# Performance work log

Hardware: AMD Instinct MI355X
Metric: run time of the kernel (lower is better)

The kernel has to match this reference:

```python
import jax, jax.numpy as jnp
import numpy as np

B, C, H, W = 4, 512, 128, 128
CI = C // 2   # inter_planes
CQ = C // 8   # q/k dim in CrossAttention


def conv1x1(x, w, b=None):
    # x: [B,Cin,H,W], w: [Cout,Cin]
    y = jnp.einsum('oc,bchw->bohw', w, x)
    if b is not None:
        y = y + b[None, :, None, None]
    return y


def setup_inputs() -> dict:
    key = jax.random.key(0)
    ks = jax.random.split(key, 13)
    s = 0.05
    return {
        'x': jax.random.normal(ks[0], (B, C, H, W), jnp.float32),
        # SCCA gating params (1x1 convs, no bias except conv_up)
        'w_q_right': jax.random.normal(ks[1], (1, C), jnp.float32) * s,
        'w_v_right': jax.random.normal(ks[2], (CI, C), jnp.float32) * s,
        'w_up': jax.random.normal(ks[3], (C, CI), jnp.float32) * s,
        'b_up': jnp.zeros((C,), jnp.float32),
        'w_q_left': jax.random.normal(ks[4], (CI, C), jnp.float32) * s,
        'w_v_left': jax.random.normal(ks[5], (CI, C), jnp.float32) * s,
        # CrossAttention params (1x1 convs with bias)
        'wq': jax.random.normal(ks[6], (CQ, C), jnp.float32) * s,
        'bq': jnp.zeros((CQ,), jnp.float32),
        'wk': jax.random.normal(ks[7], (CQ, C), jnp.float32) * s,
        'bk': jnp.zeros((CQ,), jnp.float32),
        'wv': jax.random.normal(ks[8], (C, C), jnp.float32) * s,
        'bv': jnp.zeros((C,), jnp.float32),
        'gamma': jnp.asarray(0.5, jnp.float32),
    }


def cross_attention(x, wq, bq, wk, bk, wv, bv, gamma):
    # criss-cross attention: each pixel attends to its row and column
    b, c, h, w = x.shape
    q = conv1x1(x, wq, bq)   # [B,CQ,H,W]
    k = conv1x1(x, wk, bk)   # [B,CQ,H,W]
    v = conv1x1(x, wv, bv)   # [B,C,H,W]
    # column (H) affinities with -inf on the self diagonal (as in INF())
    diag = jnp.where(jnp.eye(h, dtype=bool), -jnp.inf, 0.0).astype(x.dtype)
    e_h = jnp.einsum('bchw,bcgw->bhwg', q, k) + diag[None, :, None, :]  # [B,H,W,H]
    e_w = jnp.einsum('bchw,bchv->bhwv', q, k)                            # [B,H,W,W]
    att = jax.nn.softmax(jnp.concatenate([e_h, e_w], axis=-1), axis=-1)  # [B,H,W,H+W]
    a_h, a_w = att[..., :h], att[..., h:]
    out_h = jnp.einsum('bcgw,bhwg->bchw', v, a_h)
    out_w = jnp.einsum('bchv,bhwv->bchw', v, a_w)
    return gamma * (out_h + out_w) + x


def spatial_weighted(x, w_q_right, w_v_right, w_up, b_up):
    b, c, h, w = x.shape
    input_x = conv1x1(x, w_v_right).reshape(b, CI, h * w)       # [B,CI,HW]
    mask = jax.nn.softmax(conv1x1(x, w_q_right).reshape(b, h * w), axis=-1)  # [B,HW]
    ctx = jnp.einsum('bcn,bn->bc', input_x, mask)               # [B,CI]
    ctx = jnp.einsum('oc,bc->bo', w_up, ctx) + b_up             # [B,C]
    mask_ch = jax.nn.sigmoid(ctx)[:, :, None, None]
    return x * mask_ch


def channel_weighted(x, w_q_left, w_v_left):
    b, c, h, w = x.shape
    g_x = conv1x1(x, w_q_left)                                  # [B,CI,H,W]
    avg = g_x.mean(axis=(2, 3))                                 # [B,CI]
    theta = conv1x1(x, w_v_left).reshape(b, CI, h * w)          # [B,CI,HW]
    ctx = jax.nn.softmax(jnp.einsum('bc,bcn->bn', avg, theta), axis=-1)
    mask_sp = jax.nn.sigmoid(ctx).reshape(b, 1, h, w)
    return x * mask_sp


def reference(x, w_q_right, w_v_right, w_up, b_up, w_q_left, w_v_left,
              wq, bq, wk, bk, wv, bv, gamma):
    cc = spatial_weighted(x, w_q_right, w_v_right, w_up, b_up)
    cc = cross_attention(cc, wq, bq, wk, bk, wv, bv, gamma)
    cs = channel_weighted(x, w_q_left, w_v_left)
    cs = cross_attention(cs, wq, bq, wk, bk, wv, bv, gamma)
    out = cs + cc
    out = cross_attention(out, wq, bq, wk, bk, wv, bv, gamma)
    return out
```

## Files before the change

kernel.cpp:

```cpp
#include <hip/hip_runtime.h>
#include <hip/hip_bf16.h>
#include <math.h>

typedef __hip_bfloat16 bf16;
typedef __attribute__((ext_vector_type(8))) short s16x8;
typedef __attribute__((ext_vector_type(4))) float f32x4;

constexpr int Bn  = 4;
constexpr int Cn  = 512;
constexpr int Hn  = 128;
constexpr int Wn  = 128;
constexpr int Nn  = Hn * Wn;
constexpr int CQn = 64;
constexpr int CIn = 256;

__device__ __forceinline__ float bf2f(bf16 v){ return __bfloat162float(v); }
__device__ __forceinline__ bf16  f2bf(float v){ return __float2bfloat16(v); }

__device__ __forceinline__ void gload_lds16(const void* g, void* l){
  __builtin_amdgcn_global_load_lds(
      (const __attribute__((address_space(1))) unsigned int*)g,
      (__attribute__((address_space(3))) unsigned int*)l,
      16, 0, 0);
}


__global__ __launch_bounds__(256) void k_dotc(const float* __restrict__ x,
                                              const float* __restrict__ w,
                                              int wstride,
                                              float* __restrict__ out){
  int t = blockIdx.x * 256 + threadIdx.x;
  int b = t >> 14;
  const float* wp = w + (size_t)b * wstride;
  const float* xp = x + (size_t)b * Cn * Nn + (t & (Nn - 1));
  float acc = 0.f;
  #pragma unroll 8
  for (int c = 0; c < Cn; ++c) acc += wp[c] * xp[(size_t)c * Nn];
  out[t] = acc;
}

__global__ __launch_bounds__(256) void k_rowmean(const float* __restrict__ x,
                                                 float* __restrict__ out,
                                                 float scale){
  int bc = blockIdx.x;
  const float* xp = x + (size_t)bc * Nn;
  float acc = 0.f;
  for (int n = threadIdx.x; n < Nn; n += 256) acc += xp[n];
  for (int o = 32; o > 0; o >>= 1) acc += __shfl_down(acc, o);
  __shared__ float red[4];
  if ((threadIdx.x & 63) == 0) red[threadIdx.x >> 6] = acc;
  __syncthreads();
  if (threadIdx.x == 0) out[bc] = (red[0] + red[1] + red[2] + red[3]) * scale;
}

__global__ __launch_bounds__(256) void k_rowdot(const float* __restrict__ W,
                                                const float* __restrict__ vec,
                                                float* __restrict__ out){
  __shared__ float vs[Cn];
  int b = blockIdx.x, t = threadIdx.x;
  for (int j = t; j < Cn; j += 256) vs[j] = vec[b * Cn + j];
  __syncthreads();
  const float4* wp = (const float4*)(W + (size_t)t * Cn);
  float a = 0.f;
  #pragma unroll 4
  for (int j = 0; j < Cn / 4; ++j){
    float4 w4 = wp[j];
    a += w4.x * vs[4*j] + w4.y * vs[4*j+1] + w4.z * vs[4*j+2] + w4.w * vs[4*j+3];
  }
  out[b * CIn + t] = a;
}

__global__ __launch_bounds__(256) void k_coldot(const float* __restrict__ W,
                                                const float* __restrict__ vec,
                                                float* __restrict__ out){
  __shared__ float vs[CIn];
  int b = blockIdx.y, t = threadIdx.x;
  int c = blockIdx.x * 256 + t;
  if (t < CIn) vs[t] = vec[b * CIn + t];
  __syncthreads();
  float a = 0.f;
  #pragma unroll 8
  for (int j = 0; j < CIn; ++j) a += W[(size_t)j * Cn + c] * vs[j];
  out[b * Cn + c] = a;
}

__global__ __launch_bounds__(256) void k_mch2(const float* __restrict__ w_up,
                                              const float* __restrict__ b_up,
                                              const float* __restrict__ ctx,
                                              float* __restrict__ mch){
  __shared__ float cs[CIn];
  int b = blockIdx.y, t = threadIdx.x;
  int o = blockIdx.x * 256 + t;
  if (t < CIn) cs[t] = ctx[b * CIn + t];
  __syncthreads();
  const float4* wp = (const float4*)(w_up + (size_t)o * CIn);
  float a = b_up[o];
  #pragma unroll 4
  for (int j = 0; j < CIn / 4; ++j){
    float4 w4 = wp[j];
    a += w4.x * cs[4*j] + w4.y * cs[4*j+1] + w4.z * cs[4*j+2] + w4.w * cs[4*j+3];
  }
  mch[b * Cn + o] = 1.f / (1.f + expf(-a));
}

__global__ __launch_bounds__(1024) void k_stats(const float* __restrict__ vv,
                                                float* __restrict__ stats){
  int b = blockIdx.x;
  const float* pp = vv + (size_t)b * Nn;
  int t = threadIdx.x;
  float m = -3.4e38f;
  for (int n = t; n < Nn; n += 1024) m = fmaxf(m, pp[n]);
  for (int o = 32; o > 0; o >>= 1) m = fmaxf(m, __shfl_down(m, o));
  __shared__ float red[16];
  int wid = t >> 6, lid = t & 63;
  if (lid == 0) red[wid] = m;
  __syncthreads();
  if (t == 0){
    float q = red[0];
    for (int i = 1; i < 16; i++) q = fmaxf(q, red[i]);
    red[0] = q;
  }
  __syncthreads();
  m = red[0];
  __syncthreads();
  float s = 0.f;
  for (int n = t; n < Nn; n += 1024) s += expf(pp[n] - m);
  for (int o = 32; o > 0; o >>= 1) s += __shfl_down(s, o);
  if (lid == 0) red[wid] = s;
  __syncthreads();
  if (t == 0){
    float q = 0.f;
    for (int i = 0; i < 16; i++) q += red[i];
    stats[b * 2]     = m;
    stats[b * 2 + 1] = q;
  }
}

__global__ __launch_bounds__(256) void k_weighted(const float* __restrict__ x,
                                                  const float* __restrict__ logits,
                                                  const float* __restrict__ stats,
                                                  float* __restrict__ out){
  int bc = blockIdx.x;
  int b = bc >> 9;
  const float* xp = x + (size_t)bc * Nn;
  const float* lp = logits + (size_t)b * Nn;
  float m = stats[b * 2], den = stats[b * 2 + 1];
  float acc = 0.f;
  for (int n = threadIdx.x; n < Nn; n += 256) acc += xp[n] * expf(lp[n] - m);
  for (int o = 32; o > 0; o >>= 1) acc += __shfl_down(acc, o);
  __shared__ float red[4];
  if ((threadIdx.x & 63) == 0) red[threadIdx.x >> 6] = acc;
  __syncthreads();
  if (threadIdx.x == 0) out[bc] = (red[0] + red[1] + red[2] + red[3]) / den;
}

__global__ __launch_bounds__(256) void k_msp(const float* __restrict__ lg,
                                             const float* __restrict__ stats,
                                             float* __restrict__ msp){
  int t = blockIdx.x * 256 + threadIdx.x;
  int b = t >> 14;
  float v = expf(lg[t] - stats[b * 2]) / stats[b * 2 + 1];
  msp[t] = 1.f / (1.f + expf(-v));
}

__global__ __launch_bounds__(256) void k_applyT(const float* __restrict__ x,
                                                const float* __restrict__ mch,
                                                const float* __restrict__ msp,
                                                float* __restrict__ cc,
                                                float* __restrict__ cs,
                                                bf16* __restrict__ out_hi,
                                                bf16* __restrict__ out_lo){
  __shared__ bf16 th_[32][33];
  __shared__ bf16 tl_[32][33];
  int nt = blockIdx.x, ct = blockIdx.y, b = blockIdx.z;
  int n0 = nt * 32, c0 = ct * 32;
  int t = threadIdx.x;
  #pragma unroll
  for (int kk = 0; kk < 4; ++kk){
    int idx = t + kk * 256;
    int cl = idx >> 5, nl = idx & 31;
    size_t off = ((size_t)(b * Cn + c0 + cl)) * Nn + n0 + nl;
    float xv = x[off];
    float ccv = xv * mch[b * Cn + c0 + cl];
    float csv = xv * msp[b * Nn + n0 + nl];
    cc[off] = ccv;
    cs[off] = csv;
    bf16 h = f2bf(ccv);
    th_[cl][nl] = h;
    tl_[cl][nl] = f2bf(ccv - bf2f(h));
  }
  __syncthreads();
  #pragma unroll
  for (int kk = 0; kk < 4; ++kk){
    int idx = t + kk * 256;
    int nl = idx >> 5, cl = idx & 31;
    size_t o = ((size_t)(b * Nn + n0 + nl)) * Cn + c0 + cl;
    out_hi[o] = th_[cl][nl];
    out_lo[o] = tl_[cl][nl];
  }
}


__global__ __launch_bounds__(256) void k_cvt_w(const float* __restrict__ in,
                                               bf16* __restrict__ out, int n){
  int t = blockIdx.x * 256 + threadIdx.x;
  if (t < n) out[t] = f2bf(in[t]);
}

__global__ __launch_bounds__(256) void k_prep_wqk(const float* __restrict__ wq,
                                                  const float* __restrict__ wk,
                                                  const float* __restrict__ bq,
                                                  const float* __restrict__ bk,
                                                  bf16* __restrict__ wqk_hi,
                                                  bf16* __restrict__ wqk_lo,
                                                  float* __restrict__ bqk){
  int t = blockIdx.x * 256 + threadIdx.x;
  int o = t >> 9, c = t & 511;
  float v = (o < 64) ? wq[(size_t)o * Cn + c] : wk[(size_t)(o - 64) * Cn + c];
  bf16 h = f2bf(v);
  wqk_hi[t] = h;
  wqk_lo[t] = f2bf(v - bf2f(h));
  if (t < 128) bqk[t] = (t < 64) ? bq[t] : bk[t - 64];
}

__global__ __launch_bounds__(256) void k_cvt_T(const float* __restrict__ in,
                                               bf16* __restrict__ out_hi,
                                               bf16* __restrict__ out_lo){
  __shared__ bf16 th_[32][33];
  __shared__ bf16 tl_[32][33];
  int nt = blockIdx.x, ct = blockIdx.y, b = blockIdx.z;
  int n0 = nt * 32, c0 = ct * 32;
  int t = threadIdx.x;
  #pragma unroll
  for (int kk = 0; kk < 4; ++kk){
    int idx = t + kk * 256;
    int cl = idx >> 5, nl = idx & 31;
    float v = in[((size_t)(b * Cn + c0 + cl)) * Nn + n0 + nl];
    bf16 h = f2bf(v);
    th_[cl][nl] = h;
    tl_[cl][nl] = f2bf(v - bf2f(h));
  }
  __syncthreads();
  #pragma unroll
  for (int kk = 0; kk < 4; ++kk){
    int idx = t + kk * 256;
    int nl = idx >> 5, cl = idx & 31;
    size_t o = ((size_t)(b * Nn + n0 + nl)) * Cn + c0 + cl;
    out_hi[o] = th_[cl][nl];
    out_lo[o] = tl_[cl][nl];
  }
}


__global__ __launch_bounds__(256) void k_v_mfma(const bf16* __restrict__ xT,
                                                const bf16* __restrict__ wvb,
                                                const float* __restrict__ bv,
                                                bf16* __restrict__ v){
  __shared__ short As[128 * 64];
  __shared__ short Bs[128 * 64];
  __shared__ float bvs[128];
  int lin = blockIdx.x;
  int swz = (lin & 7) * 256 + (lin >> 3);
  int cb = (swz & 3) * 128;
  int nb = ((swz >> 2) & 127) * 128;
  int b  = swz >> 9;
  int t = threadIdx.x, lane = t & 63, wid = t >> 6;
  int wm = wid >> 1, wn = wid & 1;
  int l15 = lane & 15, l4 = lane >> 4;
  if (t < 128) bvs[t] = bv[cb + t];
  f32x4 acc[4][4];
  #pragma unroll
  for (int i = 0; i < 4; i++)
    #pragma unroll
    for (int j = 0; j < 4; j++) acc[i][j] = (f32x4){0.f, 0.f, 0.f, 0.f};

  const bf16* wp = wvb + (size_t)cb * Cn;
  const bf16* xp = xT + ((size_t)b * Nn + nb) * Cn;
  int r8 = lane >> 3;
  int kc = (lane & 7) * 8;
  for (int kt = 0; kt < 8; ++kt){
    int k0 = kt * 64;
    #pragma unroll
    for (int j = 0; j < 4; ++j){
      int inst = wid * 4 + j;
      int row = inst * 8 + r8;
      gload_lds16(wp + (size_t)row * Cn + k0 + kc, (char*)As + inst * 1024);
      gload_lds16(xp + (size_t)row * Cn + k0 + kc, (char*)Bs + inst * 1024);
    }
    __syncthreads();
    #pragma unroll
    for (int kk = 0; kk < 64; kk += 32){
      s16x8 a[4], bb[4];
      #pragma unroll
      for (int mi = 0; mi < 4; mi++)
        a[mi] = *(const s16x8*)&As[(wm * 64 + mi * 16 + l15) * 64 + kk + l4 * 8];
      #pragma unroll
      for (int ni = 0; ni < 4; ni++)
        bb[ni] = *(const s16x8*)&Bs[(wn * 64 + ni * 16 + l15) * 64 + kk + l4 * 8];
      #pragma unroll
      for (int mi = 0; mi < 4; mi++)
        #pragma unroll
        for (int ni = 0; ni < 4; ni++)
          acc[mi][ni] = __builtin_amdgcn_mfma_f32_16x16x32_bf16(a[mi], bb[ni], acc[mi][ni], 0, 0, 0);
    }
    __syncthreads();
  }
  #pragma unroll
  for (int mi = 0; mi < 4; mi++){
    #pragma unroll
    for (int r = 0; r < 4; r++){
      int cl = wm * 64 + mi * 16 + l4 * 4 + r;
      int c  = cb + cl;
      float bias = bvs[cl];
      #pragma unroll
      for (int ni = 0; ni < 4; ni++){
        int n = nb + wn * 64 + ni * 16 + l15;
        v[((size_t)(b * Cn + c)) * Nn + n] = f2bf(acc[mi][ni][r] + bias);
      }
    }
  }
}

__global__ __launch_bounds__(256) void k_qk_mfma(const bf16* __restrict__ xT_hi,
                                                 const bf16* __restrict__ xT_lo,
                                                 const bf16* __restrict__ wqk_hi,
                                                 const bf16* __restrict__ wqk_lo,
                                                 const float* __restrict__ bqk,
                                                 bf16* __restrict__ q,
                                                 bf16* __restrict__ k){
  __shared__ short Ah[128 * 64];
  __shared__ short Al[128 * 64];
  __shared__ short Bh[128 * 64];
  __shared__ short Bl[128 * 64];
  __shared__ float bs[128];
  int nb = blockIdx.x * 128, b = blockIdx.y;
  int t = threadIdx.x, lane = t & 63, wid = t >> 6;
  int wm = wid >> 1, wn = wid & 1;
  int l15 = lane & 15, l4 = lane >> 4;
  if (t < 128) bs[t] = bqk[t];
  f32x4 acc[4][4];
  #pragma unroll
  for (int i = 0; i < 4; i++)
    #pragma unroll
    for (int j = 0; j < 4; j++) acc[i][j] = (f32x4){0.f, 0.f, 0.f, 0.f};

  const bf16* xh = xT_hi + ((size_t)b * Nn + nb) * Cn;
  const bf16* xl = xT_lo + ((size_t)b * Nn + nb) * Cn;
  int r8 = lane >> 3;
  int kc = (lane & 7) * 8;
  for (int kt = 0; kt < 8; ++kt){
    int k0 = kt * 64;
    #pragma unroll
    for (int j = 0; j < 4; ++j){
      int inst = wid * 4 + j;
      int row = inst * 8 + r8;
      size_t off = (size_t)row * Cn + k0 + kc;
      gload_lds16(wqk_hi + off, (char*)Ah + inst * 1024);
      gload_lds16(wqk_lo + off, (char*)Al + inst * 1024);
      gload_lds16(xh + off,     (char*)Bh + inst * 1024);
      gload_lds16(xl + off,     (char*)Bl + inst * 1024);
    }
    __syncthreads();
    #pragma unroll
    for (int kk = 0; kk < 64; kk += 32){
      s16x8 ah[4], al[4], bh[4], bl[4];
      #pragma unroll
      for (int mi = 0; mi < 4; mi++){
        int idx = (wm * 64 + mi * 16 + l15) * 64 + kk + l4 * 8;
        ah[mi] = *(const s16x8*)&Ah[idx];
        al[mi] = *(const s16x8*)&Al[idx];
      }
      #pragma unroll
      for (int ni = 0; ni < 4; ni++){
        int idx = (wn * 64 + ni * 16 + l15) * 64 + kk + l4 * 8;
        bh[ni] = *(const s16x8*)&Bh[idx];
        bl[ni] = *(const s16x8*)&Bl[idx];
      }
      #pragma unroll
      for (int mi = 0; mi < 4; mi++)
        #pragma unroll
        for (int ni = 0; ni < 4; ni++){
          acc[mi][ni] = __builtin_amdgcn_mfma_f32_16x16x32_bf16(ah[mi], bh[ni], acc[mi][ni], 0, 0, 0);
          acc[mi][ni] = __builtin_amdgcn_mfma_f32_16x16x32_bf16(ah[mi], bl[ni], acc[mi][ni], 0, 0, 0);
          acc[mi][ni] = __builtin_amdgcn_mfma_f32_16x16x32_bf16(al[mi], bh[ni], acc[mi][ni], 0, 0, 0);
        }
    }
    __syncthreads();
  }
  #pragma unroll
  for (int mi = 0; mi < 4; mi++){
    #pragma unroll
    for (int r = 0; r < 4; r++){
      int o = wm * 64 + mi * 16 + l4 * 4 + r;
      float bias = bs[o];
      #pragma unroll
      for (int ni = 0; ni < 4; ni++){
        int n = nb + wn * 64 + ni * 16 + l15;
        float val = acc[mi][ni][r] + bias;
        if (o < 64) q[((size_t)(b * CQn + o)) * Nn + n]        = f2bf(val);
        else        k[((size_t)(b * CQn + o - 64)) * Nn + n]   = f2bf(val);
      }
    }
  }
}


__global__ __launch_bounds__(256) void k_att_h(const bf16* __restrict__ qT,
                                               const bf16* __restrict__ kT,
                                               const bf16* __restrict__ vT,
                                               float* __restrict__ mh,
                                               float* __restrict__ sh,
                                               bf16* __restrict__ ohT){
  __shared__ float smem[16384];
  float* qs = smem;
  float* ks = smem + 8192;
  char* attb = (char*)smem;
  char* vbb  = (char*)smem + 32768;
  int w = blockIdx.x, b = blockIdx.y;
  int t = threadIdx.x, lane = t & 63, wid = t >> 6;
  const bf16* qp = qT + (size_t)(b * Wn + w) * CQn * Hn;
  const bf16* kp = kT + (size_t)(b * Wn + w) * CQn * Hn;
  for (int i = t; i < 8192; i += 256){ qs[i] = bf2f(qp[i]); ks[i] = bf2f(kp[i]); }
  __syncthreads();
  int hg = t >> 3, gg = t & 7;
  float acc[4][16];
  #pragma unroll
  for (int i = 0; i < 4; i++)
    #pragma unroll
    for (int j = 0; j < 16; j++) acc[i][j] = 0.f;
  for (int c = 0; c < CQn; ++c){
    float qv[4], kv[16];
    #pragma unroll
    for (int i = 0; i < 4; i++) qv[i] = qs[c * 128 + hg * 4 + i];
    #pragma unroll
    for (int j = 0; j < 16; j++) kv[j] = ks[c * 128 + gg + 8 * j];
    #pragma unroll
    for (int i = 0; i < 4; i++)
      #pragma unroll
      for (int j = 0; j < 16; j++) acc[i][j] += qv[i] * kv[j];
  }
  float mrow[4], srow[4];
  #pragma unroll
  for (int i = 0; i < 4; i++){
    int hrow = hg * 4 + i;
    #pragma unroll
    for (int j = 0; j < 16; j++)
      if (hrow == gg + 8 * j) acc[i][j] = -1e30f;
    float m = acc[i][0];
    #pragma unroll
    for (int j = 1; j < 16; j++) m = fmaxf(m, acc[i][j]);
    m = fmaxf(m, __shfl_xor(m, 1));
    m = fmaxf(m, __shfl_xor(m, 2));
    m = fmaxf(m, __shfl_xor(m, 4));
    mrow[i] = m;
    float s = 0.f;
    #pragma unroll
    for (int j = 0; j < 16; j++){ acc[i][j] = expf(acc[i][j] - m); s += acc[i][j]; }
    s += __shfl_xor(s, 1);
    s += __shfl_xor(s, 2);
    s += __shfl_xor(s, 4);
    srow[i] = s;
  }
  __syncthreads();
  #pragma unroll
  for (int i = 0; i < 4; i++)
    #pragma unroll
    for (int j = 0; j < 16; j++){
      int h = hg * 4 + i, g = gg + 8 * j;
      bf16 bv = f2bf(acc[i][j]);
      int byte = (h * 256 + g * 2) ^ ((h & 7) << 4);
      *(unsigned short*)(attb + byte) = *(unsigned short*)&bv;
    }
  if (gg == 0){
    #pragma unroll
    for (int i = 0; i < 4; i++){
      mh[(size_t)(b * Wn + w) * Hn + hg * 4 + i] = mrow[i];
      sh[(size_t)(b * Wn + w) * Hn + hg * 4 + i] = srow[i];
    }
  }
  __syncthreads();
  int wm = wid >> 1, wn = wid & 1;
  int l15 = lane & 15, l4 = lane >> 4;
  for (int cb = 0; cb < Cn; cb += 128){
    const bf16* vp = vT + ((size_t)(b * Wn + w) * Cn + cb) * Hn;
    for (int s = t; s < 2048; s += 256){
      int row = s >> 4, seg = s & 15;
      s16x8 d = *(const s16x8*)(vp + (size_t)row * Hn + seg * 8);
      int byte = (row * 256 + seg * 16) ^ ((row & 7) << 4);
      *(s16x8*)(vbb + byte) = d;
    }
    __syncthreads();
    f32x4 acc2[4][4];
    #pragma unroll
    for (int i = 0; i < 4; i++)
      #pragma unroll
      for (int j = 0; j < 4; j++) acc2[i][j] = (f32x4){0.f, 0.f, 0.f, 0.f};
    #pragma unroll
    for (int kk = 0; kk < 128; kk += 32){
      s16x8 a[4], bb[4];
      #pragma unroll
      for (int mi = 0; mi < 4; mi++){
        int row = wm * 64 + mi * 16 + l15;
        int byte = (row * 256 + (kk + l4 * 8) * 2) ^ ((row & 7) << 4);
        a[mi] = *(const s16x8*)(vbb + byte);
      }
      #pragma unroll
      for (int ni = 0; ni < 4; ni++){
        int row = wn * 64 + ni * 16 + l15;
        int byte = (row * 256 + (kk + l4 * 8) * 2) ^ ((row & 7) << 4);
        bb[ni] = *(const s16x8*)(attb + byte);
      }
      #pragma unroll
      for (int mi = 0; mi < 4; mi++)
        #pragma unroll
        for (int ni = 0; ni < 4; ni++)
          acc2[mi][ni] = __builtin_amdgcn_mfma_f32_16x16x32_bf16(a[mi], bb[ni], acc2[mi][ni], 0, 0, 0);
    }
    bf16* op = ohT + ((size_t)(b * Wn + w) * Cn + cb) * Hn;
    #pragma unroll
    for (int mi = 0; mi < 4; mi++)
      #pragma unroll
      for (int r = 0; r < 4; r++){
        int cl = wm * 64 + mi * 16 + l4 * 4 + r;
        #pragma unroll
        for (int ni = 0; ni < 4; ni++){
          int h = wn * 64 + ni * 16 + l15;
          op[(size_t)cl * Hn + h] = f2bf(acc2[mi][ni][r]);
        }
      }
    __syncthreads();
  }
}

__global__ __launch_bounds__(256) void k_att_w(const bf16* __restrict__ q,
                                               const bf16* __restrict__ k,
                                               const bf16* __restrict__ v,
                                               float* __restrict__ mw,
                                               float* __restrict__ sw,
                                               bf16* __restrict__ ow){
  __shared__ float smem[16384];
  float* qs = smem;
  float* ks = smem + 8192;
  char* attb = (char*)smem;
  char* vbb  = (char*)smem + 32768;
  int h = blockIdx.x, b = blockIdx.y;
  int t = threadIdx.x, lane = t & 63, wid = t >> 6;
  for (int i = t; i < 8192; i += 256){
    int c = i >> 7, wl = i & 127;
    size_t base = ((size_t)(b * CQn + c) * Hn + h) * Wn + wl;
    qs[i] = bf2f(q[base]);
    ks[i] = bf2f(k[base]);
  }
  __syncthreads();
  int wg = t >> 3, vg = t & 7;
  float acc[4][16];
  #pragma unroll
  for (int i = 0; i < 4; i++)
    #pragma unroll
    for (int j = 0; j < 16; j++) acc[i][j] = 0.f;
  for (int c = 0; c < CQn; ++c){
    float qv[4], kv[16];
    #pragma unroll
    for (int i = 0; i < 4; i++) qv[i] = qs[c * 128 + wg * 4 + i];
    #pragma unroll
    for (int j = 0; j < 16; j++) kv[j] = ks[c * 128 + vg + 8 * j];
    #pragma unroll
    for (int i = 0; i < 4; i++)
      #pragma unroll
      for (int j = 0; j < 16; j++) acc[i][j] += qv[i] * kv[j];
  }
  float mrow[4], srow[4];
  #pragma unroll
  for (int i = 0; i < 4; i++){
    float m = acc[i][0];
    #pragma unroll
    for (int j = 1; j < 16; j++) m = fmaxf(m, acc[i][j]);
    m = fmaxf(m, __shfl_xor(m, 1));
    m = fmaxf(m, __shfl_xor(m, 2));
    m = fmaxf(m, __shfl_xor(m, 4));
    mrow[i] = m;
    float s = 0.f;
    #pragma unroll
    for (int j = 0; j < 16; j++){ acc[i][j] = expf(acc[i][j] - m); s += acc[i][j]; }
    s += __shfl_xor(s, 1);
    s += __shfl_xor(s, 2);
    s += __shfl_xor(s, 4);
    srow[i] = s;
  }
  __syncthreads();
  #pragma unroll
  for (int i = 0; i < 4; i++)
    #pragma unroll
    for (int j = 0; j < 16; j++){
      int wr = wg * 4 + i, g = vg + 8 * j;
      bf16 bv = f2bf(acc[i][j]);
      int byte = (wr * 256 + g * 2) ^ ((wr & 7) << 4);
      *(unsigned short*)(attb + byte) = *(unsigned short*)&bv;
    }
  if (vg == 0){
    #pragma unroll
    for (int i = 0; i < 4; i++){
      mw[(size_t)(b * Hn + h) * Wn + wg * 4 + i] = mrow[i];
      sw[(size_t)(b * Hn + h) * Wn + wg * 4 + i] = srow[i];
    }
  }
  __syncthreads();
  int wm = wid >> 1, wn = wid & 1;
  int l15 = lane & 15, l4 = lane >> 4;
  for (int cb = 0; cb < Cn; cb += 128){
    const bf16* vp = v + (size_t)(b * Cn + cb) * Nn + (size_t)h * Wn;
    for (int s = t; s < 2048; s += 256){
      int row = s >> 4, seg = s & 15;
      s16x8 d = *(const s16x8*)(vp + (size_t)row * Nn + seg * 8);
      int byte = (row * 256 + seg * 16) ^ ((row & 7) << 4);
      *(s16x8*)(vbb + byte) = d;
    }
    __syncthreads();
    f32x4 acc2[4][4];
    #pragma unroll
    for (int i = 0; i < 4; i++)
      #pragma unroll
      for (int j = 0; j < 4; j++) acc2[i][j] = (f32x4){0.f, 0.f, 0.f, 0.f};
    #pragma unroll
    for (int kk = 0; kk < 128; kk += 32){
      s16x8 a[4], bb[4];
      #pragma unroll
      for (int mi = 0; mi < 4; mi++){
        int row = wm * 64 + mi * 16 + l15;
        int byte = (row * 256 + (kk + l4 * 8) * 2) ^ ((row & 7) << 4);
        a[mi] = *(const s16x8*)(vbb + byte);
      }
      #pragma unroll
      for (int ni = 0; ni < 4; ni++){
        int row = wn * 64 + ni * 16 + l15;
        int byte = (row * 256 + (kk + l4 * 8) * 2) ^ ((row & 7) << 4);
        bb[ni] = *(const s16x8*)(attb + byte);
      }
      #pragma unroll
      for (int mi = 0; mi < 4; mi++)
        #pragma unroll
        for (int ni = 0; ni < 4; ni++)
          acc2[mi][ni] = __builtin_amdgcn_mfma_f32_16x16x32_bf16(a[mi], bb[ni], acc2[mi][ni], 0, 0, 0);
    }
    bf16* op = ow + (size_t)(b * Cn + cb) * Nn + (size_t)h * Wn;
    #pragma unroll
    for (int mi = 0; mi < 4; mi++)
      #pragma unroll
      for (int r = 0; r < 4; r++){
        int cl = wm * 64 + mi * 16 + l4 * 4 + r;
        #pragma unroll
        for (int ni = 0; ni < 4; ni++){
          int wr = wn * 64 + ni * 16 + l15;
          op[(size_t)cl * Nn + wr] = f2bf(acc2[mi][ni][r]);
        }
      }
    __syncthreads();
  }
}

__global__ __launch_bounds__(256) void k_alpha(const float* __restrict__ mh,
                                               const float* __restrict__ sh,
                                               const float* __restrict__ mw,
                                               const float* __restrict__ sw,
                                               float* __restrict__ ahT,
                                               float* __restrict__ aw){
  int t = blockIdx.x * 256 + threadIdx.x;
  int b = t >> 14;
  int hw = t & (Nn - 1);
  int h = hw >> 7, w = hw & 127;
  size_t ih = (size_t)(b * Wn + w) * Hn + h;
  size_t iw = t;
  float mhv = mh[ih], mwv = mw[iw];
  float M = fmaxf(mhv, mwv);
  float eh_ = expf(mhv - M), ew_ = expf(mwv - M);
  float inv = 1.f / (sh[ih] * eh_ + sw[iw] * ew_);
  ahT[t] = eh_ * inv;
  aw[t]  = ew_ * inv;
}


__global__ __launch_bounds__(256) void k_trans(const bf16* __restrict__ in,
                                               bf16* __restrict__ out,
                                               int CH){
  __shared__ bf16 tile[32][33];
  int tl = blockIdx.x, c = blockIdx.y, b = blockIdx.z;
  int th = tl >> 2, tw = tl & 3;
  int h0 = th * 32, w0 = tw * 32;
  int t = threadIdx.x;
  const bf16* ip = in + ((size_t)(b * CH + c)) * Nn;
  #pragma unroll
  for (int kk = 0; kk < 4; ++kk){
    int idx = t + kk * 256;
    int hl = idx >> 5, wl = idx & 31;
    tile[hl][wl] = ip[(h0 + hl) * Wn + w0 + wl];
  }
  __syncthreads();
  #pragma unroll
  for (int kk = 0; kk < 4; ++kk){
    int idx = t + kk * 256;
    int wl = idx >> 5, hl = idx & 31;
    out[((size_t)(b * Wn + w0 + wl) * CH + c) * Hn + h0 + hl] = tile[hl][wl];
  }
}

__global__ __launch_bounds__(256) void k_fuse2(const float* __restrict__ in,
                                               const bf16* __restrict__ ohT,
                                               const bf16* __restrict__ ow,
                                               const float* __restrict__ ahT,
                                               const float* __restrict__ aw,
                                               const float* __restrict__ addend,
                                               const float* __restrict__ gamma,
                                               float* __restrict__ out){
  __shared__ unsigned short tileT[128][138];
  int lin = blockIdx.x;
  int swz = (lin & 7) * 256 + (lin >> 3);
  int c = swz & 511;
  int b = swz >> 9;
  int t = threadIdx.x;
  float g = gamma[0];
  const bf16* ohp = ohT + ((size_t)(b * Wn) * Cn + c) * Hn;
  #pragma unroll
  for (int i = 0; i < 8; ++i){
    int s = t + i * 256;
    int w = s >> 4, seg = s & 15;
    s16x8 d = *(const s16x8*)(ohp + (size_t)w * (Cn * Hn) + seg * 8);
    #pragma unroll
    for (int j = 0; j < 8; ++j)
      tileT[seg * 8 + j][w] = (unsigned short)d[j];
  }
  __syncthreads();
  size_t base = ((size_t)(b * Cn + c)) * Nn;
  #pragma unroll
  for (int i = 0; i < 16; ++i){
    int o = t + i * 256;
    int h = o >> 5, w4 = (o & 31) * 4;
    size_t idx = base + (size_t)h * Wn + w4;
    size_t aidx = (size_t)b * Nn + (size_t)h * Wn + w4;
    float4 inv = *(const float4*)(in + idx);
    ushort4 owv = *(const ushort4*)((const unsigned short*)ow + idx);
    float4 ah4 = *(const float4*)(ahT + aidx);
    float4 aw4 = *(const float4*)(aw + aidx);
    float r[4];
    #pragma unroll
    for (int j = 0; j < 4; ++j){
      unsigned short uh = tileT[h][w4 + j];
      unsigned short uo = ((const unsigned short*)&owv)[j];
      float ohv = bf2f(*(bf16*)&uh);
      float owf = bf2f(*(bf16*)&uo);
      float iv  = ((const float*)&inv)[j];
      float ahv = ((const float*)&ah4)[j];
      float awv = ((const float*)&aw4)[j];
      r[j] = g * (ahv * ohv + awv * owf) + iv;
    }
    if (addend){
      float4 av = *(const float4*)(addend + idx);
      r[0] += av.x; r[1] += av.y; r[2] += av.z; r[3] += av.w;
    }
    float4 o4 = { r[0], r[1], r[2], r[3] };
    *(float4*)(out + idx) = o4;
  }
}


static void run_ca(const float* in, const bf16* wqk_hi, const bf16* wqk_lo,
                   const float* bqk, const bf16* wvb, const float* bv,
                   const float* gamma, const float* addend, float* out,
                   bf16* q, bf16* k, bf16* qT, bf16* kT, bf16* v, bf16* vT,
                   float* mh, float* sh, float* mw, float* sw, float* ahT, float* aw,
                   bf16* xT_hi, bf16* xT_lo, bf16* tmp,
                   bool do_cvt, hipStream_t stream){
  bf16* ohT = tmp;
  bf16* ow  = tmp + (size_t)Bn * Cn * Nn;
  if (do_cvt)
    k_cvt_T<<<dim3(Nn / 32, Cn / 32, Bn), 256, 0, stream>>>(in, xT_hi, xT_lo);
  k_qk_mfma<<<dim3(Nn / 128, Bn), 256, 0, stream>>>(xT_hi, xT_lo, wqk_hi, wqk_lo, bqk, q, k);
  k_trans<<<dim3(16, CQn, Bn), 256, 0, stream>>>(q, qT, CQn);
  k_trans<<<dim3(16, CQn, Bn), 256, 0, stream>>>(k, kT, CQn);
  k_v_mfma<<<2048, 256, 0, stream>>>(xT_hi, wvb, bv, v);
  k_trans<<<dim3(16, Cn, Bn), 256, 0, stream>>>(v, vT, Cn);
  k_att_h<<<dim3(Wn, Bn), 256, 0, stream>>>(qT, kT, vT, mh, sh, ohT);
  k_att_w<<<dim3(Hn, Bn), 256, 0, stream>>>(q, k, v, mw, sw, ow);
  k_alpha<<<Bn * Nn / 256, 256, 0, stream>>>(mh, sh, mw, sw, ahT, aw);
  k_fuse2<<<2048, 256, 0, stream>>>(in, ohT, ow, ahT, aw, addend, gamma, out);
}

extern "C" void kernel_launch(void* const* d_in, const int* in_sizes, int n_in,
                              void* d_out, int out_size, void* d_ws, size_t ws_size,
                              hipStream_t stream){
  (void)in_sizes; (void)n_in; (void)out_size; (void)ws_size;
  const float* x         = (const float*)d_in[0];
  const float* w_q_right = (const float*)d_in[1];
  const float* w_v_right = (const float*)d_in[2];
  const float* w_up      = (const float*)d_in[3];
  const float* b_up      = (const float*)d_in[4];
  const float* w_q_left  = (const float*)d_in[5];
  const float* w_v_left  = (const float*)d_in[6];
  const float* wq        = (const float*)d_in[7];
  const float* bq        = (const float*)d_in[8];
  const float* wk        = (const float*)d_in[9];
  const float* bk        = (const float*)d_in[10];
  const float* wv        = (const float*)d_in[11];
  const float* bv        = (const float*)d_in[12];
  const float* gamma     = (const float*)d_in[13];

  const size_t SZ_MAP = (size_t)Bn * Cn * Nn;
  char* p = (char*)d_ws;
  float* buf0   = (float*)p; p += SZ_MAP * 4;
  float* buf1   = (float*)p; p += SZ_MAP * 4;
  bf16*  vbuf   = (bf16*)p;  p += SZ_MAP * 2;
  bf16*  vT     = (bf16*)p;  p += SZ_MAP * 2;
  bf16*  qbuf   = (bf16*)p;  p += (size_t)Bn * CQn * Nn * 2;
  bf16*  kbuf   = (bf16*)p;  p += (size_t)Bn * CQn * Nn * 2;
  bf16*  qT     = (bf16*)p;  p += (size_t)Bn * CQn * Nn * 2;
  bf16*  kT     = (bf16*)p;  p += (size_t)Bn * CQn * Nn * 2;
  float* ebuf   = (float*)p; p += (size_t)SZ_MAP * 2;
  float* logits = (float*)p; p += (size_t)Bn * Nn * 4;
  float* ctxlog = (float*)p; p += (size_t)Bn * Nn * 4;
  float* msp    = (float*)p; p += (size_t)Bn * Nn * 4;
  float* xbar   = (float*)p; p += Bn * Cn * 4;
  float* wgt    = (float*)p; p += Bn * Cn * 4;
  float* u      = (float*)p; p += Bn * Cn * 4;
  float* mch    = (float*)p; p += Bn * Cn * 4;
  float* avg    = (float*)p; p += Bn * CIn * 4;
  float* ctx    = (float*)p; p += Bn * CIn * 4;
  float* stats_sp = (float*)p; p += 64;
  float* stats_ch = (float*)p; p += 64;
  bf16*  wvb    = (bf16*)p;  p += (size_t)Cn * Cn * 2;
  bf16*  wqk_hi = (bf16*)p;  p += (size_t)128 * Cn * 2;
  bf16*  wqk_lo = (bf16*)p;  p += (size_t)128 * Cn * 2;
  float* bqk    = (float*)p; p += 128 * 4;
  float* mh     = (float*)p; p += (size_t)Bn * Nn * 4;
  float* sh     = (float*)p; p += (size_t)Bn * Nn * 4;
  float* mw     = (float*)p; p += (size_t)Bn * Nn * 4;
  float* sw     = (float*)p; p += (size_t)Bn * Nn * 4;
  float* ahT    = (float*)p; p += (size_t)Bn * Nn * 4;
  float* aw     = (float*)p; p += (size_t)Bn * Nn * 4;

  bf16*  xT_hi  = (bf16*)ebuf;
  bf16*  xT_lo  = (bf16*)d_out;

  k_cvt_w<<<(Cn * Cn + 255) / 256, 256, 0, stream>>>(wv, wvb, Cn * Cn);
  k_prep_wqk<<<(128 * Cn) / 256, 256, 0, stream>>>(wq, wk, bq, bk, wqk_hi, wqk_lo, bqk);

  k_dotc<<<Bn * Nn / 256, 256, 0, stream>>>(x, w_q_right, 0, logits);
  k_rowmean<<<Bn * Cn, 256, 0, stream>>>(x, xbar, 1.f / Nn);
  k_rowdot<<<Bn, 256, 0, stream>>>(w_q_left, xbar, avg);
  k_coldot<<<dim3(Cn / 256, Bn), 256, 0, stream>>>(w_v_left, avg, u);
  k_stats<<<Bn, 1024, 0, stream>>>(logits, stats_sp);
  k_weighted<<<Bn * Cn, 256, 0, stream>>>(x, logits, stats_sp, wgt);
  k_rowdot<<<Bn, 256, 0, stream>>>(w_v_right, wgt, ctx);
  k_mch2<<<dim3(Cn / 256, Bn), 256, 0, stream>>>(w_up, b_up, ctx, mch);
  k_dotc<<<Bn * Nn / 256, 256, 0, stream>>>(x, u, Cn, ctxlog);
  k_stats<<<Bn, 1024, 0, stream>>>(ctxlog, stats_ch);
  k_msp<<<Bn * Nn / 256, 256, 0, stream>>>(ctxlog, stats_ch, msp);
  k_applyT<<<dim3(Nn / 32, Cn / 32, Bn), 256, 0, stream>>>(x, mch, msp, buf0, buf1,
                                                           xT_hi, xT_lo);

  run_ca(buf0, wqk_hi, wqk_lo, bqk, wvb, bv, gamma, nullptr, buf0,
         qbuf, kbuf, qT, kT, vbuf, vT, mh, sh, mw, sw, ahT, aw,
         xT_hi, xT_lo, (bf16*)d_out, false, stream);
  run_ca(buf1, wqk_hi, wqk_lo, bqk, wvb, bv, gamma, buf0, buf0,
         qbuf, kbuf, qT, kT, vbuf, vT, mh, sh, mw, sw, ahT, aw,
         xT_hi, xT_lo, (bf16*)d_out, true, stream);
  run_ca(buf0, wqk_hi, wqk_lo, bqk, wvb, bv, gamma, nullptr, (float*)d_out,
         qbuf, kbuf, qT, kT, vbuf, vT, mh, sh, mw, sw, ahT, aw,
         xT_hi, xT_lo, (bf16*)buf1, true, stream);
}
```

Baseline: 1.516 ms.

## Recompute masked residuals from x instead of materializing cc/cs buffers

Removes the fp32 cc and cs intermediates: the bf16 transposed inputs for each branch are built directly from x and the channel or spatial mask, and the residual in the fusion kernel is recomputed as x times the mask. The horizontal attention output is also written in channel-major [B,C,N] layout so the fusion kernel reads it contiguously. This cuts large global writes and reads, at the cost of an extra read of x for the second branch's conversion.

```diff
diff --git a/kernel.cpp b/kernel.cpp
--- a/kernel.cpp
+++ b/kernel.cpp
@@ -163,11 +163,37 @@
   msp[t] = 1.f / (1.f + expf(-v));
 }
 
-__global__ __launch_bounds__(256) void k_applyT(const float* __restrict__ x,
-                                                const float* __restrict__ mch,
+__global__ __launch_bounds__(256) void k_applyT2(const float* __restrict__ x,
+                                                 const float* __restrict__ mch,
+                                                 bf16* __restrict__ out_hi,
+                                                 bf16* __restrict__ out_lo){
+  __shared__ bf16 th_[32][33];
+  __shared__ bf16 tl_[32][33];
+  int nt = blockIdx.x, ct = blockIdx.y, b = blockIdx.z;
+  int n0 = nt * 32, c0 = ct * 32;
+  int t = threadIdx.x;
+  #pragma unroll
+  for (int kk = 0; kk < 4; ++kk){
+    int idx = t + kk * 256;
+    int cl = idx >> 5, nl = idx & 31;
+    float v = x[((size_t)(b * Cn + c0 + cl)) * Nn + n0 + nl] * mch[b * Cn + c0 + cl];
+    bf16 h = f2bf(v);
+    th_[cl][nl] = h;
+    tl_[cl][nl] = f2bf(v - bf2f(h));
+  }
+  __syncthreads();
+  #pragma unroll
+  for (int kk = 0; kk < 4; ++kk){
+    int idx = t + kk * 256;
+    int nl = idx >> 5, cl = idx & 31;
+    size_t o = ((size_t)(b * Nn + n0 + nl)) * Cn + c0 + cl;
+    out_hi[o] = th_[cl][nl];
+    out_lo[o] = tl_[cl][nl];
+  }
+}
+
+__global__ __launch_bounds__(256) void k_cvt_T2(const float* __restrict__ x,
                                                 const float* __restrict__ msp,
-                                                float* __restrict__ cc,
-                                                float* __restrict__ cs,
                                                 bf16* __restrict__ out_hi,
                                                 bf16* __restrict__ out_lo){
   __shared__ bf16 th_[32][33];
@@ -179,15 +205,10 @@
   for (int kk = 0; kk < 4; ++kk){
     int idx = t + kk * 256;
     int cl = idx >> 5, nl = idx & 31;
-    size_t off = ((size_t)(b * Cn + c0 + cl)) * Nn + n0 + nl;
-    float xv = x[off];
-    float ccv = xv * mch[b * Cn + c0 + cl];
-    float csv = xv * msp[b * Nn + n0 + nl];
-    cc[off] = ccv;
-    cs[off] = csv;
-    bf16 h = f2bf(ccv);
+    float v = x[((size_t)(b * Cn + c0 + cl)) * Nn + n0 + nl] * msp[b * Nn + n0 + nl];
+    bf16 h = f2bf(v);
     th_[cl][nl] = h;
-    tl_[cl][nl] = f2bf(ccv - bf2f(h));
+    tl_[cl][nl] = f2bf(v - bf2f(h));
   }
   __syncthreads();
   #pragma unroll
@@ -410,7 +431,7 @@
                                                const bf16* __restrict__ vT,
                                                float* __restrict__ mh,
                                                float* __restrict__ sh,
-                                               bf16* __restrict__ ohT){
+                                               bf16* __restrict__ ohX){
   __shared__ float smem[16384];
   float* qs = smem;
   float* ks = smem + 8192;
@@ -516,7 +537,7 @@
         for (int ni = 0; ni < 4; ni++)
           acc2[mi][ni] = __builtin_amdgcn_mfma_f32_16x16x32_bf16(a[mi], bb[ni], acc2[mi][ni], 0, 0, 0);
     }
-    bf16* op = ohT + ((size_t)(b * Wn + w) * Cn + cb) * Hn;
+    bf16* op = ohX + ((size_t)(b * Cn + cb)) * Nn + (size_t)w * Hn;
     #pragma unroll
     for (int mi = 0; mi < 4; mi++)
       #pragma unroll
@@ -525,7 +546,7 @@
         #pragma unroll
         for (int ni = 0; ni < 4; ni++){
           int h = wn * 64 + ni * 16 + l15;
-          op[(size_t)cl * Hn + h] = f2bf(acc2[mi][ni][r]);
+          op[(size_t)cl * Nn + h] = f2bf(acc2[mi][ni][r]);
         }
       }
     __syncthreads();
@@ -704,7 +725,9 @@
 }
 
 __global__ __launch_bounds__(256) void k_fuse2(const float* __restrict__ in,
-                                               const bf16* __restrict__ ohT,
+                                               const float* __restrict__ maskc,
+                                               const float* __restrict__ maskn,
+                                               const bf16* __restrict__ ohX,
                                                const bf16* __restrict__ ow,
                                                const float* __restrict__ ahT,
                                                const float* __restrict__ aw,
@@ -712,18 +735,16 @@
                                                const float* __restrict__ gamma,
                                                float* __restrict__ out){
   __shared__ unsigned short tileT[128][138];
-  int lin = blockIdx.x;
-  int swz = (lin & 7) * 256 + (lin >> 3);
-  int c = swz & 511;
-  int b = swz >> 9;
+  int c = blockIdx.x, b = blockIdx.y;
   int t = threadIdx.x;
   float g = gamma[0];
-  const bf16* ohp = ohT + ((size_t)(b * Wn) * Cn + c) * Hn;
+  float mc = maskc ? maskc[b * Cn + c] : 1.f;
+  const bf16* ohp = ohX + ((size_t)(b * Cn + c)) * Nn;
   #pragma unroll
   for (int i = 0; i < 8; ++i){
     int s = t + i * 256;
     int w = s >> 4, seg = s & 15;
-    s16x8 d = *(const s16x8*)(ohp + (size_t)w * (Cn * Hn) + seg * 8);
+    s16x8 d = *(const s16x8*)(ohp + (size_t)s * 8);
     #pragma unroll
     for (int j = 0; j < 8; ++j)
       tileT[seg * 8 + j][w] = (unsigned short)d[j];
@@ -740,6 +761,7 @@
     ushort4 owv = *(const ushort4*)((const unsigned short*)ow + idx);
     float4 ah4 = *(const float4*)(ahT + aidx);
     float4 aw4 = *(const float4*)(aw + aidx);
+    float4 mn4 = maskn ? *(const float4*)(maskn + aidx) : (float4){1.f,1.f,1.f,1.f};
     float r[4];
     #pragma unroll
     for (int j = 0; j < 4; ++j){
@@ -747,7 +769,7 @@
       unsigned short uo = ((const unsigned short*)&owv)[j];
       float ohv = bf2f(*(bf16*)&uh);
       float owf = bf2f(*(bf16*)&uo);
-      float iv  = ((const float*)&inv)[j];
+      float iv  = ((const float*)&inv)[j] * mc * ((const float*)&mn4)[j];
       float ahv = ((const float*)&ah4)[j];
       float awv = ((const float*)&aw4)[j];
       r[j] = g * (ahv * ohv + awv * owf) + iv;
@@ -762,26 +784,25 @@
 }
 
 
-static void run_ca(const float* in, const bf16* wqk_hi, const bf16* wqk_lo,
+static void run_ca(const float* resid, const float* maskc, const float* maskn,
+                   const bf16* wqk_hi, const bf16* wqk_lo,
                    const float* bqk, const bf16* wvb, const float* bv,
                    const float* gamma, const float* addend, float* out,
                    bf16* q, bf16* k, bf16* qT, bf16* kT, bf16* v, bf16* vT,
                    float* mh, float* sh, float* mw, float* sw, float* ahT, float* aw,
-                   bf16* xT_hi, bf16* xT_lo, bf16* tmp,
-                   bool do_cvt, hipStream_t stream){
-  bf16* ohT = tmp;
+                   bf16* xT_hi, bf16* xT_lo, bf16* tmp, hipStream_t stream){
+  bf16* ohX = tmp;
   bf16* ow  = tmp + (size_t)Bn * Cn * Nn;
-  if (do_cvt)
-    k_cvt_T<<<dim3(Nn / 32, Cn / 32, Bn), 256, 0, stream>>>(in, xT_hi, xT_lo);
   k_qk_mfma<<<dim3(Nn / 128, Bn), 256, 0, stream>>>(xT_hi, xT_lo, wqk_hi, wqk_lo, bqk, q, k);
   k_trans<<<dim3(16, CQn, Bn), 256, 0, stream>>>(q, qT, CQn);
   k_trans<<<dim3(16, CQn, Bn), 256, 0, stream>>>(k, kT, CQn);
   k_v_mfma<<<2048, 256, 0, stream>>>(xT_hi, wvb, bv, v);
   k_trans<<<dim3(16, Cn, Bn), 256, 0, stream>>>(v, vT, Cn);
-  k_att_h<<<dim3(Wn, Bn), 256, 0, stream>>>(qT, kT, vT, mh, sh, ohT);
+  k_att_h<<<dim3(Wn, Bn), 256, 0, stream>>>(qT, kT, vT, mh, sh, ohX);
   k_att_w<<<dim3(Hn, Bn), 256, 0, stream>>>(q, k, v, mw, sw, ow);
   k_alpha<<<Bn * Nn / 256, 256, 0, stream>>>(mh, sh, mw, sw, ahT, aw);
-  k_fuse2<<<2048, 256, 0, stream>>>(in, ohT, ow, ahT, aw, addend, gamma, out);
+  k_fuse2<<<dim3(Cn, Bn), 256, 0, stream>>>(resid, maskc, maskn, ohX, ow, ahT, aw,
+                                            addend, gamma, out);
 }
 
 extern "C" void kernel_launch(void* const* d_in, const int* in_sizes, int n_in,
@@ -853,16 +874,18 @@
   k_dotc<<<Bn * Nn / 256, 256, 0, stream>>>(x, u, Cn, ctxlog);
   k_stats<<<Bn, 1024, 0, stream>>>(ctxlog, stats_ch);
   k_msp<<<Bn * Nn / 256, 256, 0, stream>>>(ctxlog, stats_ch, msp);
-  k_applyT<<<dim3(Nn / 32, Cn / 32, Bn), 256, 0, stream>>>(x, mch, msp, buf0, buf1,
-                                                           xT_hi, xT_lo);
-
-  run_ca(buf0, wqk_hi, wqk_lo, bqk, wvb, bv, gamma, nullptr, buf0,
+
+  k_applyT2<<<dim3(Nn / 32, Cn / 32, Bn), 256, 0, stream>>>(x, mch, xT_hi, xT_lo);
+  run_ca(x, mch, nullptr, wqk_hi, wqk_lo, bqk, wvb, bv, gamma, nullptr, buf0,
          qbuf, kbuf, qT, kT, vbuf, vT, mh, sh, mw, sw, ahT, aw,
-         xT_hi, xT_lo, (bf16*)d_out, false, stream);
-  run_ca(buf1, wqk_hi, wqk_lo, bqk, wvb, bv, gamma, buf0, buf0,
+         xT_hi, xT_lo, (bf16*)d_out, stream);
+  k_cvt_T2<<<dim3(Nn / 32, Cn / 32, Bn), 256, 0, stream>>>(x, msp, xT_hi, xT_lo);
+  run_ca(x, nullptr, msp, wqk_hi, wqk_lo, bqk, wvb, bv, gamma, buf0, buf0,
          qbuf, kbuf, qT, kT, vbuf, vT, mh, sh, mw, sw, ahT, aw,
-         xT_hi, xT_lo, (bf16*)d_out, true, stream);
-  run_ca(buf0, wqk_hi, wqk_lo, bqk, wvb, bv, gamma, nullptr, (float*)d_out,
+         xT_hi, xT_lo, (bf16*)d_out, stream);
+  k_cvt_T<<<dim3(Nn / 32, Cn / 32, Bn), 256, 0, stream>>>(buf0, xT_hi, xT_lo);
+  run_ca(buf0, nullptr, nullptr, wqk_hi, wqk_lo, bqk, wvb, bv, gamma, nullptr,
+         (float*)d_out,
          qbuf, kbuf, qT, kT, vbuf, vT, mh, sh, mw, sw, ahT, aw,
-         xT_hi, xT_lo, (bf16*)buf1, true, stream);
-}
+         xT_hi, xT_lo, (bf16*)buf1, stream);
+}
```

Measured after the change: 1.400 ms. 1.08x faster.
